# Kernel tuning notes

Hardware: AMD Instinct MI355X
Metric: run time of the kernel (lower is better)

Reference implementation:

```python
import jax, jax.numpy as jnp
import numpy as np

N = 50000      # nodes
E = 800000     # edges
F = 128        # num_features
D = 64         # dim
G = 512        # graphs
L = 3          # num_gc_layers
ITERS = 2      # summary_iter
BN_EPS = 1e-5


def setup_inputs() -> dict:
    key = jax.random.key(0)
    ks = jax.random.split(key, 40)
    rn = lambda k, shp, s=0.1: jax.random.normal(k, shp, dtype=jnp.float32) * s
    inp = {}
    inp["x"] = jax.random.normal(ks[0], (N, F), dtype=jnp.float32)
    inp["edge_index"] = jax.random.randint(ks[1], (2, E), 0, N)
    inp["batch"] = jnp.sort(jax.random.randint(ks[2], (N,), 0, G))
    inp["noise"] = rn(ks[3], (N, D), 1.0)
    # GIN layer 0 MLP (F->D->D), layers 1..2 MLPs (D->D->D) stacked
    inp["W1_0"] = rn(ks[4], (F, D)); inp["b1_0"] = jnp.zeros((D,), jnp.float32)
    inp["W2_0"] = rn(ks[5], (D, D)); inp["b2_0"] = jnp.zeros((D,), jnp.float32)
    inp["W1_r"] = rn(ks[6], (L - 1, D, D)); inp["b1_r"] = jnp.zeros((L - 1, D), jnp.float32)
    inp["W2_r"] = rn(ks[7], (L - 1, D, D)); inp["b2_r"] = jnp.zeros((L - 1, D), jnp.float32)
    inp["bn_gamma"] = jnp.ones((L, D), jnp.float32)
    inp["bn_beta"] = jnp.zeros((L, D), jnp.float32)
    # Summary_Maker: slot-attention-style iterative pooling with a GRUCell
    inp["Wq"] = rn(ks[8], (D, D)); inp["Wk"] = rn(ks[9], (D, D)); inp["Wv"] = rn(ks[10], (D, D))
    inp["gru_Wih"] = rn(ks[11], (3 * D, D)); inp["gru_Whh"] = rn(ks[12], (3 * D, D))
    inp["gru_bih"] = jnp.zeros((3 * D,), jnp.float32); inp["gru_bhh"] = jnp.zeros((3 * D,), jnp.float32)
    # projection heads
    inp["node_mu_W"] = rn(ks[13], (D, D)); inp["node_mu_b"] = jnp.zeros((D,), jnp.float32)
    inp["node_lv_W"] = rn(ks[14], (D, D)); inp["node_lv_b"] = jnp.zeros((D,), jnp.float32)
    inp["graph_mu_W"] = rn(ks[15], (D, D)); inp["graph_mu_b"] = jnp.zeros((D,), jnp.float32)
    inp["graph_lv_W"] = rn(ks[16], (D, D)); inp["graph_lv_b"] = jnp.zeros((D,), jnp.float32)
    inp["proj_bn_gamma"] = jnp.ones((4, D), jnp.float32)
    inp["proj_bn_beta"] = jnp.zeros((4, D), jnp.float32)
    return inp


def batchnorm(h, g, b):
    m = h.mean(0)
    v = h.var(0)  # biased, matching torch BatchNorm1d normalization in train mode
    return (h - m) * jax.lax.rsqrt(v + BN_EPS) * g + b


def gin_layer(h, src, dst, W1, b1, W2, b2, gamma, beta):
    # GINConv(eps=0): nn(x_i + sum_{j->i} x_j); messages gathered at src, scattered to dst
    agg = h + jax.ops.segment_sum(h[src], dst, num_segments=N)
    z = jax.nn.relu(agg @ W1 + b1) @ W2 + b2
    return batchnorm(jax.nn.relu(z), gamma, beta)


def gru_cell(u, h, Wih, Whh, bih, bhh):
    gi = u @ Wih.T + bih
    gh = h @ Whh.T + bhh
    i_r, i_z, i_n = jnp.split(gi, 3, axis=-1)
    h_r, h_z, h_n = jnp.split(gh, 3, axis=-1)
    r = jax.nn.sigmoid(i_r + h_r)
    z = jax.nn.sigmoid(i_z + h_z)
    n = jnp.tanh(i_n + r * h_n)
    return (1.0 - z) * n + z * h


def segment_softmax(logits, seg, num_segments):
    m = jax.ops.segment_max(logits, seg, num_segments=num_segments)
    e = jnp.exp(logits - m[seg])
    s = jax.ops.segment_sum(e, seg, num_segments=num_segments)
    return e / (s[seg] + 1e-9)


def summary_maker(h, batch, noise, Wq, Wk, Wv, Wih, Whh, bih, bhh):
    cnt = jnp.maximum(jax.ops.segment_sum(jnp.ones((N,), h.dtype), batch, num_segments=G), 1.0)
    slots = jax.ops.segment_sum(h, batch, num_segments=G) / cnt[:, None]  # mean init
    k = h @ Wk
    v = h @ Wv
    scale = 1.0 / np.sqrt(D)
    attn = jnp.zeros((N,), h.dtype)
    for _ in range(ITERS):
        q = slots @ Wq
        logits = (k * q[batch]).sum(-1) * scale  # [N]
        attn = segment_softmax(logits, batch, G)
        updates = jax.ops.segment_sum(attn[:, None] * v, batch, num_segments=G)
        slots = gru_cell(updates, slots, Wih, Whh, bih, bhh)
    summary_related = attn[:, None] * h          # [N, D]
    noisy = summary_related + noise              # [N, D]
    return slots, summary_related, noisy


def reference(x, edge_index, batch, noise,
              W1_0, b1_0, W2_0, b2_0, W1_r, b1_r, W2_r, b2_r, bn_gamma, bn_beta,
              Wq, Wk, Wv, gru_Wih, gru_Whh, gru_bih, gru_bhh,
              node_mu_W, node_mu_b, node_lv_W, node_lv_b,
              graph_mu_W, graph_mu_b, graph_lv_W, graph_lv_b,
              proj_bn_gamma, proj_bn_beta):
    src, dst = edge_index[0], edge_index[1]
    h = gin_layer(x, src, dst, W1_0, b1_0, W2_0, b2_0, bn_gamma[0], bn_beta[0])
    for i in range(L - 1):
        h = gin_layer(h, src, dst, W1_r[i], b1_r[i], W2_r[i], b2_r[i], bn_gamma[i + 1], bn_beta[i + 1])
    slots, _srni, noisy = summary_maker(h, batch, noise, Wq, Wk, Wv, gru_Wih, gru_Whh, gru_bih, gru_bhh)
    node_mu = batchnorm(jax.nn.relu(noisy @ node_mu_W + node_mu_b), proj_bn_gamma[0], proj_bn_beta[0])
    node_lv = batchnorm(jax.nn.relu(noisy @ node_lv_W + node_lv_b), proj_bn_gamma[1], proj_bn_beta[1])
    graph_mu = batchnorm(jax.nn.relu(slots @ graph_mu_W + graph_mu_b), proj_bn_gamma[2], proj_bn_beta[2])
    graph_lv = batchnorm(jax.nn.relu(slots @ graph_lv_W + graph_lv_b), proj_bn_gamma[3], proj_bn_beta[3])
    return (node_mu, node_lv, graph_mu, graph_lv)
```

## Files before the change

### kernel.cpp

```cpp
#include <hip/hip_runtime.h>

#define NN 50000
#define EE 800000
#define FF 128
#define DD 64
#define GG 512

typedef unsigned short u16;


__device__ __forceinline__ float bf2f(u16 h) {
    unsigned u = ((unsigned)h) << 16;
    return __builtin_bit_cast(float, u);
}
__device__ __forceinline__ u16 f2bf(float f) {
    unsigned u = __builtin_bit_cast(unsigned, f);
    u += 0x7fffu + ((u >> 16) & 1u);
    return (u16)(u >> 16);
}
__device__ __forceinline__ float4 ldbf4(const u16* p) {
    uint2 v = *(const uint2*)p;
    float4 r;
    r.x = bf2f((u16)(v.x & 0xffffu)); r.y = bf2f((u16)(v.x >> 16));
    r.z = bf2f((u16)(v.y & 0xffffu)); r.w = bf2f((u16)(v.y >> 16));
    return r;
}
__device__ __forceinline__ void stbf4(u16* p, float4 v) {
    uint2 o;
    o.x = (unsigned)f2bf(v.x) | ((unsigned)f2bf(v.y) << 16);
    o.y = (unsigned)f2bf(v.z) | ((unsigned)f2bf(v.w) << 16);
    *(uint2*)p = o;
}
__device__ __forceinline__ void fma4(float4& a, const float4& w, float s) {
    a.x = fmaf(s, w.x, a.x); a.y = fmaf(s, w.y, a.y);
    a.z = fmaf(s, w.z, a.z); a.w = fmaf(s, w.w, a.w);
}
__device__ __forceinline__ void add4(float4& a, float4 b) {
    a.x += b.x; a.y += b.y; a.z += b.z; a.w += b.w;
}

__device__ __forceinline__ void gather16(float4& acc, const u16* __restrict__ in,
                                         const u16* __restrict__ csr, int e0s, int e1s,
                                         int l16, int gbase) {
    for (int e0 = e0s; e0 < e1s; e0 += 16) {
        int cnt = min(16, e1s - e0);
        int srcv = (l16 < cnt) ? (int)csr[e0 + l16] : 0;
        int j = 0;
        for (; j + 8 <= cnt; j += 8) {
            int i0 = __shfl(srcv, gbase + j);
            int i1 = __shfl(srcv, gbase + j + 1);
            int i2 = __shfl(srcv, gbase + j + 2);
            int i3 = __shfl(srcv, gbase + j + 3);
            int i4 = __shfl(srcv, gbase + j + 4);
            int i5 = __shfl(srcv, gbase + j + 5);
            int i6 = __shfl(srcv, gbase + j + 6);
            int i7 = __shfl(srcv, gbase + j + 7);
            float4 h0 = ldbf4(in + (size_t)i0 * 64 + l16 * 4);
            float4 h1 = ldbf4(in + (size_t)i1 * 64 + l16 * 4);
            float4 h2 = ldbf4(in + (size_t)i2 * 64 + l16 * 4);
            float4 h3 = ldbf4(in + (size_t)i3 * 64 + l16 * 4);
            float4 h4 = ldbf4(in + (size_t)i4 * 64 + l16 * 4);
            float4 h5 = ldbf4(in + (size_t)i5 * 64 + l16 * 4);
            float4 h6 = ldbf4(in + (size_t)i6 * 64 + l16 * 4);
            float4 h7 = ldbf4(in + (size_t)i7 * 64 + l16 * 4);
            add4(h0, h1); add4(h2, h3); add4(h4, h5); add4(h6, h7);
            add4(h0, h2); add4(h4, h6);
            add4(h0, h4);
            add4(acc, h0);
        }
        for (; j + 4 <= cnt; j += 4) {
            int i0 = __shfl(srcv, gbase + j);
            int i1 = __shfl(srcv, gbase + j + 1);
            int i2 = __shfl(srcv, gbase + j + 2);
            int i3 = __shfl(srcv, gbase + j + 3);
            float4 h0 = ldbf4(in + (size_t)i0 * 64 + l16 * 4);
            float4 h1 = ldbf4(in + (size_t)i1 * 64 + l16 * 4);
            float4 h2 = ldbf4(in + (size_t)i2 * 64 + l16 * 4);
            float4 h3 = ldbf4(in + (size_t)i3 * 64 + l16 * 4);
            add4(h0, h1); add4(h2, h3); add4(h0, h2);
            add4(acc, h0);
        }
        for (; j < cnt; ++j) {
            int s = __shfl(srcv, gbase + j);
            float4 hv = ldbf4(in + (size_t)s * 64 + l16 * 4);
            add4(acc, hv);
        }
    }
}


__global__ void zero_all_k(int* __restrict__ cursor, float* __restrict__ stats_all) {
    int i = blockIdx.x * blockDim.x + threadIdx.x;
    if (i < NN) cursor[i] = 0;
    if (i < 7 * 128) stats_all[i] = 0.f;
}


__global__ void hist_k(const int* __restrict__ dst, int* __restrict__ deg) {
    int e = (blockIdx.x * 256 + threadIdx.x) * 2;
    if (e + 2 <= EE) {
        int2 d = *(const int2*)&dst[e];
        atomicAdd(&deg[d.x], 1); atomicAdd(&deg[d.y], 1);
    } else {
        for (; e < EE; ++e) atomicAdd(&deg[dst[e]], 1);
    }
}

__global__ __launch_bounds__(1024) void scanA_k(const int* __restrict__ deg,
                                                int* __restrict__ rowstart,
                                                int* __restrict__ blocksum) {
    __shared__ int buf[1024];
    int tid = threadIdx.x;
    int base = blockIdx.x * 1024;
    int v = (base + tid < NN) ? deg[base + tid] : 0;
    buf[tid] = v;
    __syncthreads();
    for (int o = 1; o < 1024; o <<= 1) {
        int t = (tid >= o) ? buf[tid - o] : 0;
        __syncthreads();
        buf[tid] += t;
        __syncthreads();
    }
    if (base + tid < NN) rowstart[base + tid + 1] = buf[tid];
    if (tid == 1023) blocksum[blockIdx.x] = buf[1023];
}

__global__ void scanB_k(const int* __restrict__ blocksum, int* __restrict__ bofs, int nb) {
    int lane = threadIdx.x;
    int v = (lane < nb) ? blocksum[lane] : 0;
    int orig = v;
    for (int o = 1; o < 64; o <<= 1) {
        int t = __shfl_up(v, o);
        if (lane >= o) v += t;
    }
    if (lane < nb) bofs[lane] = v - orig;
}

__global__ void scanC_k(int* __restrict__ rowstart, const int* __restrict__ bofs,
                        int* __restrict__ cursor) {
    int i = blockIdx.x * blockDim.x + threadIdx.x;
    if (i >= NN) return;
    int val = rowstart[i + 1] + bofs[i >> 10];
    rowstart[i + 1] = val;
    if (i + 1 < NN) cursor[i + 1] = val;
    if (i == 0) { rowstart[0] = 0; cursor[0] = 0; }
}

__global__ void fill_k(const int* __restrict__ src, const int* __restrict__ dst,
                       int* __restrict__ cursor, u16* __restrict__ csr16) {
    int e = (blockIdx.x * 256 + threadIdx.x) * 2;
    if (e + 2 <= EE) {
        int2 d = *(const int2*)&dst[e];
        int2 s = *(const int2*)&src[e];
        int p0 = atomicAdd(&cursor[d.x], 1);
        int p1 = atomicAdd(&cursor[d.y], 1);
        csr16[p0] = (u16)s.x; csr16[p1] = (u16)s.y;
    } else {
        for (; e < EE; ++e) { int p = atomicAdd(&cursor[dst[e]], 1); csr16[p] = (u16)src[e]; }
    }
}


__global__ void seg_bounds_k(const int* __restrict__ batch, int* __restrict__ segstart) {
    int g = blockIdx.x * blockDim.x + threadIdx.x;
    if (g > GG) return;
    int lo = 0, hi = NN;
    while (lo < hi) {
        int mid = (lo + hi) >> 1;
        if (batch[mid] < g) lo = mid + 1; else hi = mid;
    }
    segstart[g] = lo;
}


__global__ __launch_bounds__(256) void agg_gemm_k(
    const u16* __restrict__ in,
    const int* __restrict__ rowstart, const u16* __restrict__ csr,
    const float* __restrict__ bias1,
    const float* __restrict__ W2, const float* __restrict__ bias2,
    u16* __restrict__ out, float* __restrict__ gstats)
{
    constexpr int KP = 68;
    __shared__ float sW[64 * 64];
    __shared__ float sIn[64 * KP];
    __shared__ float sStat[128];
    const int tid = threadIdx.x;

    for (int i = tid; i < 64 * 16; i += 256) ((float4*)sW)[i] = ((const float4*)W2)[i];

    const int tile = blockIdx.x * 64;
    const int nrows = min(64, NN - tile);
    const int l16 = tid & 15, gbase = tid & 48, grp = tid >> 4;
    float4 b1v = ((const float4*)bias1)[l16];
    for (int r = grp; r < nrows; r += 16) {
        int node = tile + r;
        float4 acc = ldbf4(in + (size_t)node * 64 + l16 * 4);
        gather16(acc, in, csr, rowstart[node], rowstart[node + 1], l16, gbase);
        acc.x = fmaxf(acc.x + b1v.x, 0.f); acc.y = fmaxf(acc.y + b1v.y, 0.f);
        acc.z = fmaxf(acc.z + b1v.z, 0.f); acc.w = fmaxf(acc.w + b1v.w, 0.f);
        *(float4*)&sIn[r * KP + l16 * 4] = acc;
    }
    __syncthreads();

    const int rg = (tid >> 4) * 4, c0 = (tid & 15) << 2;
    float4 bb = *(const float4*)&bias2[c0];
    float4 acc[4];
#pragma unroll
    for (int j = 0; j < 4; ++j) acc[j] = bb;
#pragma unroll 2
    for (int k4 = 0; k4 < 16; ++k4) {
        float4 av[4];
#pragma unroll
        for (int j = 0; j < 4; ++j) av[j] = *(const float4*)&sIn[(rg + j) * KP + k4 * 4];
        const float* wp = &sW[k4 * 4 * 64 + c0];
        float4 w0 = *(const float4*)(wp);
        float4 w1 = *(const float4*)(wp + 64);
        float4 w2 = *(const float4*)(wp + 128);
        float4 w3 = *(const float4*)(wp + 192);
#pragma unroll
        for (int j = 0; j < 4; ++j) {
            fma4(acc[j], w0, av[j].x); fma4(acc[j], w1, av[j].y);
            fma4(acc[j], w2, av[j].z); fma4(acc[j], w3, av[j].w);
        }
    }
#pragma unroll
    for (int j = 0; j < 4; ++j) {
        acc[j].x = fmaxf(acc[j].x, 0.f); acc[j].y = fmaxf(acc[j].y, 0.f);
        acc[j].z = fmaxf(acc[j].z, 0.f); acc[j].w = fmaxf(acc[j].w, 0.f);
        if (rg + j < nrows) stbf4(out + (size_t)(tile + rg + j) * 64 + c0, acc[j]);
    }
    if (tid < 128) sStat[tid] = 0.f;
    __syncthreads();
    float sx = 0, sy = 0, sz = 0, sw = 0, qx = 0, qy = 0, qz = 0, qw = 0;
#pragma unroll
    for (int j = 0; j < 4; ++j) {
        if (rg + j < nrows) {
            sx += acc[j].x; sy += acc[j].y; sz += acc[j].z; sw += acc[j].w;
            qx += acc[j].x * acc[j].x; qy += acc[j].y * acc[j].y;
            qz += acc[j].z * acc[j].z; qw += acc[j].w * acc[j].w;
        }
    }
    atomicAdd(&sStat[c0 + 0], sx); atomicAdd(&sStat[c0 + 1], sy);
    atomicAdd(&sStat[c0 + 2], sz); atomicAdd(&sStat[c0 + 3], sw);
    atomicAdd(&sStat[64 + c0 + 0], qx); atomicAdd(&sStat[64 + c0 + 1], qy);
    atomicAdd(&sStat[64 + c0 + 2], qz); atomicAdd(&sStat[64 + c0 + 3], qw);
    __syncthreads();
    if (tid < 128) atomicAdd(&gstats[tid], sStat[tid]);
}


__global__ __launch_bounds__(256) void fused_layer_k(
    const u16* __restrict__ in,
    const int* __restrict__ rowstart, const u16* __restrict__ csr,
    const float* __restrict__ bnst, const float* __restrict__ gam, const float* __restrict__ bet,
    const float* __restrict__ W1, const float* __restrict__ b1,
    const float* __restrict__ W2, const float* __restrict__ b2,
    u16* __restrict__ out, float* __restrict__ gstats)
{
    constexpr int KP = 68;
    __shared__ float sW[64 * 64];
    __shared__ float sAgg[64 * KP];
    __shared__ float sStat[128];
    __shared__ float aL[64], dL[64];
    const int tid = threadIdx.x;

    for (int i = tid; i < 64 * 16; i += 256) ((float4*)sW)[i] = ((const float4*)W1)[i];
    if (tid < 64) {
        float m = bnst[tid] * (1.f / NN);
        float v = bnst[64 + tid] * (1.f / NN) - m * m;
        float a = rsqrtf(v + 1e-5f) * gam[tid];
        aL[tid] = a;
        dL[tid] = bet[tid] - m * a;
    }
    __syncthreads();

    const int tile = blockIdx.x * 64;
    const int nrows = min(64, NN - tile);
    const int l16 = tid & 15, gbase = tid & 48, grp = tid >> 4;
    float4 av4 = *(const float4*)&aL[l16 * 4];
    float4 dv4 = *(const float4*)&dL[l16 * 4];
    for (int r = grp; r < nrows; r += 16) {
        int node = tile + r;
        int e0s = rowstart[node], e1s = rowstart[node + 1];
        float4 acc = ldbf4(in + (size_t)node * 64 + l16 * 4);
        gather16(acc, in, csr, e0s, e1s, l16, gbase);
        float dp1 = (float)(e1s - e0s + 1);
        acc.x = fmaf(av4.x, acc.x, dp1 * dv4.x);
        acc.y = fmaf(av4.y, acc.y, dp1 * dv4.y);
        acc.z = fmaf(av4.z, acc.z, dp1 * dv4.z);
        acc.w = fmaf(av4.w, acc.w, dp1 * dv4.w);
        *(float4*)&sAgg[r * KP + l16 * 4] = acc;
    }
    __syncthreads();

    const int rg = (tid >> 4) * 4, c0 = (tid & 15) << 2;
    float4 t[4];
    {
        float4 bb = *(const float4*)&b1[c0];
#pragma unroll
        for (int j = 0; j < 4; ++j) t[j] = bb;
#pragma unroll 2
        for (int k4 = 0; k4 < 16; ++k4) {
            float4 a0[4];
#pragma unroll
            for (int j = 0; j < 4; ++j) a0[j] = *(const float4*)&sAgg[(rg + j) * KP + k4 * 4];
            const float* wp = &sW[k4 * 4 * 64 + c0];
            float4 w0 = *(const float4*)(wp);
            float4 w1 = *(const float4*)(wp + 64);
            float4 w2 = *(const float4*)(wp + 128);
            float4 w3 = *(const float4*)(wp + 192);
#pragma unroll
            for (int j = 0; j < 4; ++j) {
                fma4(t[j], w0, a0[j].x); fma4(t[j], w1, a0[j].y);
                fma4(t[j], w2, a0[j].z); fma4(t[j], w3, a0[j].w);
            }
        }
#pragma unroll
        for (int j = 0; j < 4; ++j) {
            t[j].x = fmaxf(t[j].x, 0.f); t[j].y = fmaxf(t[j].y, 0.f);
            t[j].z = fmaxf(t[j].z, 0.f); t[j].w = fmaxf(t[j].w, 0.f);
        }
    }
    __syncthreads();

    for (int i = tid; i < 64 * 16; i += 256) ((float4*)sW)[i] = ((const float4*)W2)[i];
#pragma unroll
    for (int j = 0; j < 4; ++j) *(float4*)&sAgg[(rg + j) * KP + c0] = t[j];
    __syncthreads();

    float4 acc[4];
    {
        float4 bb = *(const float4*)&b2[c0];
#pragma unroll
        for (int j = 0; j < 4; ++j) acc[j] = bb;
#pragma unroll 2
        for (int k4 = 0; k4 < 16; ++k4) {
            float4 a0[4];
#pragma unroll
            for (int j = 0; j < 4; ++j) a0[j] = *(const float4*)&sAgg[(rg + j) * KP + k4 * 4];
            const float* wp = &sW[k4 * 4 * 64 + c0];
            float4 w0 = *(const float4*)(wp);
            float4 w1 = *(const float4*)(wp + 64);
            float4 w2 = *(const float4*)(wp + 128);
            float4 w3 = *(const float4*)(wp + 192);
#pragma unroll
            for (int j = 0; j < 4; ++j) {
                fma4(acc[j], w0, a0[j].x); fma4(acc[j], w1, a0[j].y);
                fma4(acc[j], w2, a0[j].z); fma4(acc[j], w3, a0[j].w);
            }
        }
    }
#pragma unroll
    for (int j = 0; j < 4; ++j) {
        acc[j].x = fmaxf(acc[j].x, 0.f); acc[j].y = fmaxf(acc[j].y, 0.f);
        acc[j].z = fmaxf(acc[j].z, 0.f); acc[j].w = fmaxf(acc[j].w, 0.f);
        if (rg + j < nrows) stbf4(out + (size_t)(tile + rg + j) * 64 + c0, acc[j]);
    }
    if (tid < 128) sStat[tid] = 0.f;
    __syncthreads();
    float sx = 0, sy = 0, sz = 0, sw = 0, qx = 0, qy = 0, qz = 0, qw = 0;
#pragma unroll
    for (int j = 0; j < 4; ++j) {
        if (rg + j < nrows) {
            sx += acc[j].x; sy += acc[j].y; sz += acc[j].z; sw += acc[j].w;
            qx += acc[j].x * acc[j].x; qy += acc[j].y * acc[j].y;
            qz += acc[j].z * acc[j].z; qw += acc[j].w * acc[j].w;
        }
    }
    atomicAdd(&sStat[c0 + 0], sx); atomicAdd(&sStat[c0 + 1], sy);
    atomicAdd(&sStat[c0 + 2], sz); atomicAdd(&sStat[c0 + 3], sw);
    atomicAdd(&sStat[64 + c0 + 0], qx); atomicAdd(&sStat[64 + c0 + 1], qy);
    atomicAdd(&sStat[64 + c0 + 2], qz); atomicAdd(&sStat[64 + c0 + 3], qw);
    __syncthreads();
    if (tid < 128) atomicAdd(&gstats[tid], sStat[tid]);
}


template<int K, bool BIAS, bool RELU, bool STATS, bool ROWSCALE, bool BNIN, bool DUAL,
         bool INBF, bool OUTBF>
__global__ __launch_bounds__(256) void gemm_k(
    const void* __restrict__ in, const float* __restrict__ W, const float* __restrict__ Wb,
    const float* __restrict__ bias, const float* __restrict__ bias2,
    void* __restrict__ out, void* __restrict__ out2, int rows,
    float* __restrict__ gstats, float* __restrict__ gstats2,
    const float* __restrict__ attn, const float* __restrict__ noise,
    const float* __restrict__ bnstats, const float* __restrict__ gamma,
    const float* __restrict__ beta)
{
    constexpr int RPT = (K == 128) ? 2 : 4;
    constexpr int TR  = 16 * RPT;
    constexpr int KP  = K + 4;
    constexpr int SS  = DUAL ? 256 : 128;
    __shared__ float sW[K * 64];
    __shared__ float sWb[DUAL ? K * 64 : 4];
    __shared__ float sIn[TR * KP];
    __shared__ float sStat[STATS ? SS : 4];
    __shared__ float sA[BNIN ? 64 : 4];
    __shared__ float sD[BNIN ? 64 : 4];

    const int tid = threadIdx.x;
    for (int i = tid; i < K * 16; i += 256) ((float4*)sW)[i] = ((const float4*)W)[i];
    if (DUAL)
        for (int i = tid; i < K * 16; i += 256) ((float4*)sWb)[i] = ((const float4*)Wb)[i];
    if (BNIN && tid < 64) {
        float m   = bnstats[tid] * (1.f / NN);
        float v   = bnstats[64 + tid] * (1.f / NN) - m * m;
        float a   = rsqrtf(v + 1e-5f) * gamma[tid];
        sA[tid] = a;
        sD[tid] = beta[tid] - m * a;
    }

    int rg = (tid >> 4) * RPT;
    int c0 = (tid & 15) << 2;
    float4 bb  = make_float4(0.f, 0.f, 0.f, 0.f);
    float4 bb2 = make_float4(0.f, 0.f, 0.f, 0.f);
    if (BIAS) bb = *(const float4*)&bias[c0];
    if (BIAS && DUAL) bb2 = *(const float4*)&bias2[c0];

    for (int tile = blockIdx.x * TR; tile < rows; tile += gridDim.x * TR) {
        __syncthreads();
        int nrows = min(TR, rows - tile);
        const float4* igf = INBF ? nullptr : (const float4*)((const float*)in + (size_t)tile * K);
        const u16*    igb = INBF ? ((const u16*)in + (size_t)tile * K) : nullptr;
        const float4* ng  = ROWSCALE ? (const float4*)(noise + (size_t)tile * K) : nullptr;
        for (int i = tid; i < nrows * (K / 4); i += 256) {
            int rr = i / (K / 4), kk = (i - rr * (K / 4)) * 4;
            float4 t = INBF ? ldbf4(igb + i * 4) : igf[i];
            if (BNIN) {
                t.x = fmaf(sA[kk + 0], t.x, sD[kk + 0]);
                t.y = fmaf(sA[kk + 1], t.y, sD[kk + 1]);
                t.z = fmaf(sA[kk + 2], t.z, sD[kk + 2]);
                t.w = fmaf(sA[kk + 3], t.w, sD[kk + 3]);
            }
            if (ROWSCALE) {
                float4 nv = ng[i];
                float at = attn[tile + rr];
                t.x = fmaf(at, t.x, nv.x); t.y = fmaf(at, t.y, nv.y);
                t.z = fmaf(at, t.z, nv.z); t.w = fmaf(at, t.w, nv.w);
            }
            *(float4*)&sIn[rr * KP + kk] = t;
        }
        __syncthreads();

        float4 acc[RPT];
        float4 acc2[DUAL ? RPT : 1];
#pragma unroll
        for (int j = 0; j < RPT; ++j) acc[j] = bb;
        if (DUAL) {
#pragma unroll
            for (int j = 0; j < RPT; ++j) acc2[j] = bb2;
        }
#pragma unroll 2
        for (int k4 = 0; k4 < K / 4; ++k4) {
            float4 av[RPT];
#pragma unroll
            for (int j = 0; j < RPT; ++j)
                av[j] = *(const float4*)&sIn[(rg + j) * KP + k4 * 4];
            const float* wp = &sW[k4 * 4 * 64 + c0];
            float4 w0 = *(const float4*)(wp);
            float4 w1 = *(const float4*)(wp + 64);
            float4 w2 = *(const float4*)(wp + 128);
            float4 w3 = *(const float4*)(wp + 192);
#pragma unroll
            for (int j = 0; j < RPT; ++j) {
                fma4(acc[j], w0, av[j].x); fma4(acc[j], w1, av[j].y);
                fma4(acc[j], w2, av[j].z); fma4(acc[j], w3, av[j].w);
            }
            if (DUAL) {
                const float* wq = &sWb[k4 * 4 * 64 + c0];
                float4 u0 = *(const float4*)(wq);
                float4 u1 = *(const float4*)(wq + 64);
                float4 u2 = *(const float4*)(wq + 128);
                float4 u3 = *(const float4*)(wq + 192);
#pragma unroll
                for (int j = 0; j < RPT; ++j) {
                    fma4(acc2[j], u0, av[j].x); fma4(acc2[j], u1, av[j].y);
                    fma4(acc2[j], u2, av[j].z); fma4(acc2[j], u3, av[j].w);
                }
            }
        }
        if (RELU) {
#pragma unroll
            for (int j = 0; j < RPT; ++j) {
                acc[j].x = fmaxf(acc[j].x, 0.f); acc[j].y = fmaxf(acc[j].y, 0.f);
                acc[j].z = fmaxf(acc[j].z, 0.f); acc[j].w = fmaxf(acc[j].w, 0.f);
                if (DUAL) {
                    acc2[j].x = fmaxf(acc2[j].x, 0.f); acc2[j].y = fmaxf(acc2[j].y, 0.f);
                    acc2[j].z = fmaxf(acc2[j].z, 0.f); acc2[j].w = fmaxf(acc2[j].w, 0.f);
                }
            }
        }
#pragma unroll
        for (int j = 0; j < RPT; ++j) {
            int r = rg + j;
            if (r < nrows) {
                if (OUTBF) stbf4((u16*)out + (size_t)(tile + r) * 64 + c0, acc[j]);
                else *(float4*)((float*)out + (size_t)(tile + r) * 64 + c0) = acc[j];
                if (DUAL) {
                    if (OUTBF) stbf4((u16*)out2 + (size_t)(tile + r) * 64 + c0, acc2[j]);
                    else *(float4*)((float*)out2 + (size_t)(tile + r) * 64 + c0) = acc2[j];
                }
            }
        }
        if (STATS) {
            if (tid < SS) sStat[tid] = 0.f;
            __syncthreads();
            float sx = 0, sy = 0, sz = 0, sw = 0, qx = 0, qy = 0, qz = 0, qw = 0;
            float sx2 = 0, sy2 = 0, sz2 = 0, sw2 = 0, qx2 = 0, qy2 = 0, qz2 = 0, qw2 = 0;
#pragma unroll
            for (int j = 0; j < RPT; ++j) {
                if (rg + j < nrows) {
                    sx += acc[j].x; sy += acc[j].y; sz += acc[j].z; sw += acc[j].w;
                    qx += acc[j].x * acc[j].x; qy += acc[j].y * acc[j].y;
                    qz += acc[j].z * acc[j].z; qw += acc[j].w * acc[j].w;
                    if (DUAL) {
                        sx2 += acc2[j].x; sy2 += acc2[j].y; sz2 += acc2[j].z; sw2 += acc2[j].w;
                        qx2 += acc2[j].x * acc2[j].x; qy2 += acc2[j].y * acc2[j].y;
                        qz2 += acc2[j].z * acc2[j].z; qw2 += acc2[j].w * acc2[j].w;
                    }
                }
            }
            atomicAdd(&sStat[c0 + 0], sx); atomicAdd(&sStat[c0 + 1], sy);
            atomicAdd(&sStat[c0 + 2], sz); atomicAdd(&sStat[c0 + 3], sw);
            atomicAdd(&sStat[64 + c0 + 0], qx); atomicAdd(&sStat[64 + c0 + 1], qy);
            atomicAdd(&sStat[64 + c0 + 2], qz); atomicAdd(&sStat[64 + c0 + 3], qw);
            if (DUAL) {
                atomicAdd(&sStat[128 + c0 + 0], sx2); atomicAdd(&sStat[128 + c0 + 1], sy2);
                atomicAdd(&sStat[128 + c0 + 2], sz2); atomicAdd(&sStat[128 + c0 + 3], sw2);
                atomicAdd(&sStat[192 + c0 + 0], qx2); atomicAdd(&sStat[192 + c0 + 1], qy2);
                atomicAdd(&sStat[192 + c0 + 2], qz2); atomicAdd(&sStat[192 + c0 + 3], qw2);
            }
            __syncthreads();
            if (tid < 128) atomicAdd(&gstats[tid], sStat[tid]);
            if (DUAL && tid >= 128) atomicAdd(&gstats2[tid - 128], sStat[tid]);
        }
    }
}


__global__ void bn_apply2b_k(const u16* __restrict__ in1, const u16* __restrict__ in2,
                             float* __restrict__ out1, float* __restrict__ out2, int rows,
                             const float* __restrict__ st1, const float* __restrict__ st2,
                             const float* __restrict__ g1, const float* __restrict__ b1,
                             const float* __restrict__ g2, const float* __restrict__ b2) {
    int n = rows * 64;
    float invr = 1.f / (float)rows;
    for (int i = blockIdx.x * blockDim.x + threadIdx.x; i < n; i += gridDim.x * blockDim.x) {
        int c = i & 63;
        float m1 = st1[c] * invr;
        float v1 = st1[64 + c] * invr - m1 * m1;
        out1[i] = (bf2f(in1[i]) - m1) * rsqrtf(v1 + 1e-5f) * g1[c] + b1[c];
        float m2 = st2[c] * invr;
        float v2 = st2[64 + c] * invr - m2 * m2;
        out2[i] = (bf2f(in2[i]) - m2) * rsqrtf(v2 + 1e-5f) * g2[c] + b2[c];
    }
}


__global__ void bn_apply2_k(const float* __restrict__ in1, const float* __restrict__ in2,
                            float* __restrict__ out1, float* __restrict__ out2, int rows,
                            const float* __restrict__ st1, const float* __restrict__ st2,
                            const float* __restrict__ g1, const float* __restrict__ b1,
                            const float* __restrict__ g2, const float* __restrict__ b2) {
    int n = rows * 64;
    float invr = 1.f / (float)rows;
    for (int i = blockIdx.x * blockDim.x + threadIdx.x; i < n; i += gridDim.x * blockDim.x) {
        int c = i & 63;
        float m1 = st1[c] * invr;
        float v1 = st1[64 + c] * invr - m1 * m1;
        out1[i] = (in1[i] - m1) * rsqrtf(v1 + 1e-5f) * g1[c] + b1[c];
        float m2 = st2[c] * invr;
        float v2 = st2[64 + c] * invr - m2 * m2;
        out2[i] = (in2[i] - m2) * rsqrtf(v2 + 1e-5f) * g2[c] + b2[c];
    }
}


__global__ __launch_bounds__(512) void attn3_k(
    const u16* __restrict__ z, const int* __restrict__ segst,
    const float* __restrict__ bnst, const float* __restrict__ gam, const float* __restrict__ bet,
    const float* __restrict__ Wq, const float* __restrict__ Wk, const float* __restrict__ Wv,
    const float* __restrict__ Wih, const float* __restrict__ Whh,
    const float* __restrict__ bih, const float* __restrict__ bhh,
    float* __restrict__ attn, float* __restrict__ slots_out)
{
    int g = blockIdx.x, tid = threadIdx.x, w = tid >> 6, lane = tid & 63;
    __shared__ float ssl[64], sq[64], swr[64], sm[64], supd[64], sred[512], ssum[8];
    __shared__ float aL[64], dL[64];
    __shared__ float sgi[192], sgh[192];
    __shared__ float sc, sinv;

    int s0 = segst[g], s1 = segst[g + 1];
    if (tid < 64) {
        float m = bnst[tid] * (1.f / NN);
        float v = bnst[64 + tid] * (1.f / NN) - m * m;
        float a = rsqrtf(v + 1e-5f) * gam[tid];
        aL[tid] = a;
        dL[tid] = bet[tid] - m * a;
    }
    __syncthreads();

    {
        float macc = 0.f;
        for (int n = s0 + w; n < s1; n += 8) macc += bf2f(z[(size_t)n * 64 + lane]);
        sred[tid] = macc;
        __syncthreads();
        if (tid < 64) {
            float s = 0.f;
#pragma unroll
            for (int k = 0; k < 8; ++k) s += sred[tid + 64 * k];
            ssl[tid] = fmaf(aL[tid], s / (float)max(s1 - s0, 1), dL[tid]);
        }
        __syncthreads();
    }

    for (int it = 0; it < 2; ++it) {
        {
            float p = 0.f;
#pragma unroll
            for (int kk = 0; kk < 8; ++kk) p += ssl[w * 8 + kk] * Wq[(w * 8 + kk) * 64 + lane];
            sred[tid] = p;
        }
        __syncthreads();
        if (tid < 64) {
            float s = 0.f;
#pragma unroll
            for (int k = 0; k < 8; ++k) s += sred[tid + 64 * k];
            sq[tid] = s;
        }
        __syncthreads();
        {
            float p = 0.f;
#pragma unroll
            for (int kk = 0; kk < 8; ++kk) p += Wk[lane * 64 + w * 8 + kk] * sq[w * 8 + kk];
            sred[tid] = p;
        }
        __syncthreads();
        if (tid < 64) {
            float s = 0.f;
#pragma unroll
            for (int k = 0; k < 8; ++k) s += sred[tid + 64 * k];
            swr[tid] = s;
        }
        __syncthreads();
        if (tid < 64) {
            float pr = dL[tid] * swr[tid];
            pr += __shfl_xor(pr, 1);  pr += __shfl_xor(pr, 2);  pr += __shfl_xor(pr, 4);
            pr += __shfl_xor(pr, 8);  pr += __shfl_xor(pr, 16); pr += __shfl_xor(pr, 32);
            if (tid == 0) sc = pr * 0.125f;
            swr[tid] = aL[tid] * swr[tid] * 0.125f;
        }
        __syncthreads();
        float wl = swr[lane], cc = sc;

        float s = 0.f, u = 0.f;
        for (int n = s0 + w; n < s1; n += 8) {
            float zl = bf2f(z[(size_t)n * 64 + lane]);
            float l = zl * wl;
            l += __shfl_xor(l, 1);  l += __shfl_xor(l, 2);  l += __shfl_xor(l, 4);
            l += __shfl_xor(l, 8);  l += __shfl_xor(l, 16); l += __shfl_xor(l, 32);
            float e = expf(l + cc);
            if (lane == 0) attn[n] = e;
            s += e;
            u = fmaf(e, zl, u);
        }
        sred[tid] = u;
        if (lane == 0) ssum[w] = s;
        __syncthreads();
        if (tid < 64) {
            float stot = ssum[0] + ssum[1] + ssum[2] + ssum[3]
                       + ssum[4] + ssum[5] + ssum[6] + ssum[7] + 1e-9f;
            if (tid == 0) sinv = 1.f / stot;
            float uu = 0.f;
#pragma unroll
            for (int k = 0; k < 8; ++k) uu += sred[tid + 64 * k];
            sm[tid] = fmaf(aL[tid], uu / stot, dL[tid]);
        }
        __syncthreads();
        {
            float p = 0.f;
#pragma unroll
            for (int kk = 0; kk < 8; ++kk) p += sm[w * 8 + kk] * Wv[(w * 8 + kk) * 64 + lane];
            sred[tid] = p;
        }
        __syncthreads();
        if (tid < 64) {
            float s2 = 0.f;
#pragma unroll
            for (int k = 0; k < 8; ++k) s2 += sred[tid + 64 * k];
            supd[tid] = s2;
        }
        __syncthreads();

        if (it == 1) {
            float inv = sinv;
            for (int n = s0 + tid; n < s1; n += 512) attn[n] *= inv;
        }

        if (tid < 192) {
            float a = bih[tid], b = bhh[tid];
            const float* wi = &Wih[tid * 64];
            const float* wh = &Whh[tid * 64];
#pragma unroll 8
            for (int j = 0; j < 64; ++j) { a += supd[j] * wi[j]; b += ssl[j] * wh[j]; }
            sgi[tid] = a; sgh[tid] = b;
        }
        __syncthreads();
        if (tid < 64) {
            float r  = 1.f / (1.f + expf(-(sgi[tid] + sgh[tid])));
            float zz = 1.f / (1.f + expf(-(sgi[64 + tid] + sgh[64 + tid])));
            float nn = tanhf(sgi[128 + tid] + r * sgh[128 + tid]);
            float ns = (1.f - zz) * nn + zz * ssl[tid];
            ssl[tid] = ns;
            if (it == 1) slots_out[g * 64 + tid] = ns;
        }
        __syncthreads();
    }
}


extern "C" void kernel_launch(void* const* d_in, const int* in_sizes, int n_in,
                              void* d_out, int out_size, void* d_ws, size_t ws_size,
                              hipStream_t stream) {
    (void)in_sizes; (void)n_in; (void)out_size; (void)ws_size;

    const float* x      = (const float*)d_in[0];
    const int*   ei     = (const int*)d_in[1];
    const int*   srcI   = ei;
    const int*   dstI   = ei + EE;
    const int*   batch  = (const int*)d_in[2];
    const float* noise  = (const float*)d_in[3];
    const float* W1_0   = (const float*)d_in[4];
    const float* b1_0   = (const float*)d_in[5];
    const float* W2_0   = (const float*)d_in[6];
    const float* b2_0   = (const float*)d_in[7];
    const float* W1_r   = (const float*)d_in[8];
    const float* b1_r   = (const float*)d_in[9];
    const float* W2_r   = (const float*)d_in[10];
    const float* b2_r   = (const float*)d_in[11];
    const float* bn_g   = (const float*)d_in[12];
    const float* bn_b   = (const float*)d_in[13];
    const float* Wq     = (const float*)d_in[14];
    const float* Wk     = (const float*)d_in[15];
    const float* Wv     = (const float*)d_in[16];
    const float* Wih    = (const float*)d_in[17];
    const float* Whh    = (const float*)d_in[18];
    const float* bih    = (const float*)d_in[19];
    const float* bhh    = (const float*)d_in[20];
    const float* nmW    = (const float*)d_in[21];
    const float* nmb    = (const float*)d_in[22];
    const float* nlW    = (const float*)d_in[23];
    const float* nlb    = (const float*)d_in[24];
    const float* gmW    = (const float*)d_in[25];
    const float* gmb    = (const float*)d_in[26];
    const float* glW    = (const float*)d_in[27];
    const float* glb    = (const float*)d_in[28];
    const float* pj_g   = (const float*)d_in[29];
    const float* pj_b   = (const float*)d_in[30];

    char* w = (char*)d_ws;
    u16*   B0b   = (u16*)w;            w += (size_t)NN * 64 * 2;
    u16*   B1b   = (u16*)w;            w += (size_t)NN * 64 * 2;
    u16*   B2b   = (u16*)w;            w += (size_t)NN * 64 * 2;
    float* slots = (float*)w;          w += GG * 64 * 4;
    float* gpre1 = (float*)w;          w += GG * 64 * 4;
    float* gpre2 = (float*)w;          w += GG * 64 * 4;
    float* attn  = (float*)w;          w += NN * 4;
    float* stats = (float*)w;          w += 7 * 128 * 4;
    int*   segst = (int*)w;            w += (GG + 1) * 4;
    int*   rowst = (int*)w;            w += (NN + 1) * 4;
    int*   cursor= (int*)w;            w += NN * 4;
    int*   bsum  = (int*)w;            w += 64 * 4;
    int*   bofs  = (int*)w;            w += 64 * 4;
    u16*   csr16 = (u16*)w;            w += (size_t)EE * 2;

    float* s0 = stats, *s1 = stats + 128, *s2 = stats + 256, *s3 = stats + 384,
         * s4 = stats + 512, *s5 = stats + 640, *s6 = stats + 768;

    float* outp = (float*)d_out;
    float* out_nmu = outp;
    float* out_nlv = outp + NN * DD;
    float* out_gmu = outp + 2 * NN * DD;
    float* out_glv = outp + 2 * NN * DD + GG * DD;

    constexpr int NB = (NN + 1023) / 1024;
    constexpr int GE2 = (EE / 2 + 255) / 256;
    constexpr int NT64 = (NN + 63) / 64;
    const float* np = nullptr;
    float* zp = nullptr;

#define GK(...) <<<__VA_ARGS__, 0, stream>>>
    zero_all_k GK((NN + 255) / 256, 256)(cursor, stats);
    hist_k GK(GE2, 256)(dstI, cursor);
    scanA_k GK(NB, 1024)(cursor, rowst, bsum);
    scanB_k GK(1, 64)(bsum, bofs, NB);
    scanC_k GK((NN + 255) / 256, 256)(rowst, bofs, cursor);
    fill_k GK(GE2, 256)(srcI, dstI, cursor, csr16);
    seg_bounds_k GK(3, 256)(batch, segst);

    gemm_k<128,false,false,false,false,false,false,false,true> GK(1563, 256)
        (x, W1_0, np, np, np, B0b, zp, NN, zp, zp, np, np, np, np, np);
    agg_gemm_k GK(NT64, 256)(B0b, rowst, csr16, b1_0, W2_0, b2_0, B1b, s0);

    fused_layer_k GK(NT64, 256)(B1b, rowst, csr16, s0, bn_g + 0, bn_b + 0,
                                W1_r, b1_r, W2_r, b2_r, B2b, s1);
    fused_layer_k GK(NT64, 256)(B2b, rowst, csr16, s1, bn_g + 64, bn_b + 64,
                                W1_r + DD * DD, b1_r + DD, W2_r + DD * DD, b2_r + DD, B0b, s2);

    attn3_k GK(GG, 512)(B0b, segst, s2, bn_g + 128, bn_b + 128,
                        Wq, Wk, Wv, Wih, Whh, bih, bhh, attn, slots);

    gemm_k<64,true,true,true,true,true,true,true,true> GK(782, 256)
        (B0b, nmW, nlW, nmb, nlb, B1b, B2b, NN, s3, s4, attn, noise, s2, bn_g + 128, bn_b + 128);
    bn_apply2b_k GK(2048, 256)(B1b, B2b, out_nmu, out_nlv, NN, s3, s4,
                               pj_g + 0, pj_b + 0, pj_g + 64, pj_b + 64);

    gemm_k<64,true,true,true,false,false,true,false,false> GK(8, 256)
        (slots, gmW, glW, gmb, glb, gpre1, gpre2, GG, s5, s6, np, np, np, np, np);
    bn_apply2_k GK(128, 256)(gpre1, gpre2, out_gmu, out_glv, GG, s5, s6,
                             pj_g + 128, pj_b + 128, pj_g + 192, pj_b + 192);
#undef GK
}
```

Baseline: 381.3 us.

## Fold segment-bound search into init, widen edge kernels, add dedicated first-layer GEMM

Merges the segment-bounds binary search into the zeroing kernel, removing one launch. The histogram and CSR fill kernels now process four edges per thread through int4 loads, so fewer threads issue wider loads. The generic first-layer GEMM is replaced by a dedicated kernel that keeps W1_0 in shared memory as bf16 and computes 16 rows per block with fp32 accumulation. Rounding W1_0 to bf16 may shift numerics slightly, and each of the many small blocks repeats the weight staging.

Result: no change. 385.0 us (+1.0%).

```diff
diff --git a/kernel.cpp b/kernel.cpp
--- a/kernel.cpp
+++ b/kernel.cpp
@@ -20,6 +20,12 @@
 }
 __device__ __forceinline__ float4 ldbf4(const u16* p) {
     uint2 v = *(const uint2*)p;
+    float4 r;
+    r.x = bf2f((u16)(v.x & 0xffffu)); r.y = bf2f((u16)(v.x >> 16));
+    r.z = bf2f((u16)(v.y & 0xffffu)); r.w = bf2f((u16)(v.y >> 16));
+    return r;
+}
+__device__ __forceinline__ float4 bfu2f4(uint2 v) {
     float4 r;
     r.x = bf2f((u16)(v.x & 0xffffu)); r.y = bf2f((u16)(v.x >> 16));
     r.z = bf2f((u16)(v.y & 0xffffu)); r.w = bf2f((u16)(v.y >> 16));
@@ -89,18 +95,28 @@
 }
 
 
-__global__ void zero_all_k(int* __restrict__ cursor, float* __restrict__ stats_all) {
+__global__ void init_k(int* __restrict__ cursor, float* __restrict__ stats_all,
+                       const int* __restrict__ batch, int* __restrict__ segstart) {
     int i = blockIdx.x * blockDim.x + threadIdx.x;
     if (i < NN) cursor[i] = 0;
     if (i < 7 * 128) stats_all[i] = 0.f;
+    if (i <= GG) {
+        int lo = 0, hi = NN;
+        while (lo < hi) {
+            int mid = (lo + hi) >> 1;
+            if (batch[mid] < i) lo = mid + 1; else hi = mid;
+        }
+        segstart[i] = lo;
+    }
 }
 
 
 __global__ void hist_k(const int* __restrict__ dst, int* __restrict__ deg) {
-    int e = (blockIdx.x * 256 + threadIdx.x) * 2;
-    if (e + 2 <= EE) {
-        int2 d = *(const int2*)&dst[e];
+    int e = (blockIdx.x * 256 + threadIdx.x) * 4;
+    if (e + 4 <= EE) {
+        int4 d = *(const int4*)&dst[e];
         atomicAdd(&deg[d.x], 1); atomicAdd(&deg[d.y], 1);
+        atomicAdd(&deg[d.z], 1); atomicAdd(&deg[d.w], 1);
     } else {
         for (; e < EE; ++e) atomicAdd(&deg[dst[e]], 1);
     }
@@ -148,28 +164,57 @@
 
 __global__ void fill_k(const int* __restrict__ src, const int* __restrict__ dst,
                        int* __restrict__ cursor, u16* __restrict__ csr16) {
-    int e = (blockIdx.x * 256 + threadIdx.x) * 2;
-    if (e + 2 <= EE) {
-        int2 d = *(const int2*)&dst[e];
-        int2 s = *(const int2*)&src[e];
+    int e = (blockIdx.x * 256 + threadIdx.x) * 4;
+    if (e + 4 <= EE) {
+        int4 d = *(const int4*)&dst[e];
+        int4 s = *(const int4*)&src[e];
         int p0 = atomicAdd(&cursor[d.x], 1);
         int p1 = atomicAdd(&cursor[d.y], 1);
+        int p2 = atomicAdd(&cursor[d.z], 1);
+        int p3 = atomicAdd(&cursor[d.w], 1);
         csr16[p0] = (u16)s.x; csr16[p1] = (u16)s.y;
+        csr16[p2] = (u16)s.z; csr16[p3] = (u16)s.w;
     } else {
         for (; e < EE; ++e) { int p = atomicAdd(&cursor[dst[e]], 1); csr16[p] = (u16)src[e]; }
     }
 }
 
 
-__global__ void seg_bounds_k(const int* __restrict__ batch, int* __restrict__ segstart) {
-    int g = blockIdx.x * blockDim.x + threadIdx.x;
-    if (g > GG) return;
-    int lo = 0, hi = NN;
-    while (lo < hi) {
-        int mid = (lo + hi) >> 1;
-        if (batch[mid] < g) lo = mid + 1; else hi = mid;
-    }
-    segstart[g] = lo;
+__global__ __launch_bounds__(256) void gemm128_k(const float* __restrict__ x,
+                                                 const float* __restrict__ W,
+                                                 u16* __restrict__ out) {
+    __shared__ u16 sW16[128 * 64];
+    __shared__ float sIn[16 * 132];
+    const int tid = threadIdx.x;
+    for (int i = tid * 4; i < 128 * 64; i += 1024) {
+        float4 w = *(const float4*)(W + i);
+        uint2 pk;
+        pk.x = (unsigned)f2bf(w.x) | ((unsigned)f2bf(w.y) << 16);
+        pk.y = (unsigned)f2bf(w.z) | ((unsigned)f2bf(w.w) << 16);
+        *(uint2*)&sW16[i] = pk;
+    }
+    const int tile = blockIdx.x * 16;
+    const int nrows = min(16, NN - tile);
+    for (int i = tid; i < 16 * 32; i += 256) {
+        int rr = i >> 5, kk = (i & 31) * 4;
+        float4 t = (rr < nrows) ? *(const float4*)(x + (size_t)(tile + rr) * 128 + kk)
+                                : make_float4(0.f, 0.f, 0.f, 0.f);
+        *(float4*)&sIn[rr * 132 + kk] = t;
+    }
+    __syncthreads();
+    int rg = tid >> 4, c0 = (tid & 15) << 2;
+    float4 acc = make_float4(0.f, 0.f, 0.f, 0.f);
+#pragma unroll 4
+    for (int k4 = 0; k4 < 32; ++k4) {
+        float4 av = *(const float4*)&sIn[rg * 132 + k4 * 4];
+        float as[4] = {av.x, av.y, av.z, av.w};
+#pragma unroll
+        for (int kk = 0; kk < 4; ++kk) {
+            uint2 wp = *(const uint2*)&sW16[(k4 * 4 + kk) * 64 + c0];
+            fma4(acc, bfu2f4(wp), as[kk]);
+        }
+    }
+    if (rg < nrows) stbf4(out + (size_t)(tile + rg) * 64 + c0, acc);
 }
 
 
@@ -784,22 +829,20 @@
     float* out_glv = outp + 2 * NN * DD + GG * DD;
 
     constexpr int NB = (NN + 1023) / 1024;
-    constexpr int GE2 = (EE / 2 + 255) / 256;
+    constexpr int GE4 = (EE / 4 + 255) / 256;
     constexpr int NT64 = (NN + 63) / 64;
+    constexpr int NT16 = (NN + 15) / 16;
     const float* np = nullptr;
-    float* zp = nullptr;
 
 #define GK(...) <<<__VA_ARGS__, 0, stream>>>
-    zero_all_k GK((NN + 255) / 256, 256)(cursor, stats);
-    hist_k GK(GE2, 256)(dstI, cursor);
+    init_k GK((NN + 255) / 256, 256)(cursor, stats, batch, segst);
+    hist_k GK(GE4, 256)(dstI, cursor);
     scanA_k GK(NB, 1024)(cursor, rowst, bsum);
     scanB_k GK(1, 64)(bsum, bofs, NB);
     scanC_k GK((NN + 255) / 256, 256)(rowst, bofs, cursor);
-    fill_k GK(GE2, 256)(srcI, dstI, cursor, csr16);
-    seg_bounds_k GK(3, 256)(batch, segst);
-
-    gemm_k<128,false,false,false,false,false,false,false,true> GK(1563, 256)
-        (x, W1_0, np, np, np, B0b, zp, NN, zp, zp, np, np, np, np, np);
+    fill_k GK(GE4, 256)(srcI, dstI, cursor, csr16);
+
+    gemm128_k GK(NT16, 256)(x, W1_0, B0b);
     agg_gemm_k GK(NT64, 256)(B0b, rowst, csr16, b1_0, W2_0, b2_0, B1b, s0);
 
     fused_layer_k GK(NT64, 256)(B1b, rowst, csr16, s0, bn_g + 0, bn_b + 0,
```
